# Kernel optimization log

Measured on AMD Instinct MI355X. Metric: run time of the kernel, lower is better.

Reference implementation:

```python
import jax, jax.numpy as jnp
import numpy as np

B, S, D, H, R = 2, 2048, 1024, 16, 4
HD = D // H  # 64


def _linear_params(key, din, dout):
    k1, k2 = jax.random.split(key)
    bound = 1.0 / np.sqrt(din)
    w = jax.random.uniform(k1, (din, dout), jnp.float32, -bound, bound)
    b = jax.random.uniform(k2, (dout,), jnp.float32, -bound, bound)
    return w, b


def setup_inputs() -> dict:
    key = jax.random.key(0)
    ks = jax.random.split(key, 10)
    x = jax.random.normal(ks[0], (B, S, D), jnp.float32)
    wq_p, bq_p = _linear_params(ks[1], D, D)
    wk_p, bk_p = _linear_params(ks[2], D, D)
    wv_p, bv_p = _linear_params(ks[3], D, D)
    wo_p, bo_p = _linear_params(ks[4], D, D)
    wq_s, bq_s = _linear_params(ks[5], D, H * R)
    wk_s, bk_s = _linear_params(ks[6], D, H * R)
    wv_s, bv_s = _linear_params(ks[7], D, H * R)
    wo_s, bo_s = _linear_params(ks[8], H * R, D)
    w_cross = jnp.float32(-0.1)
    return {"x": x,
            "wq_p": wq_p, "bq_p": bq_p, "wk_p": wk_p, "bk_p": bk_p,
            "wv_p": wv_p, "bv_p": bv_p, "wo_p": wo_p, "bo_p": bo_p,
            "wq_s": wq_s, "bq_s": bq_s, "wk_s": wk_s, "bk_s": bk_s,
            "wv_s": wv_s, "bv_s": bv_s, "wo_s": wo_s, "bo_s": bo_s,
            "w_cross": w_cross}


def _mha(x, wq, bq, wk, bk, wv, bv, dh, scale):
    b, s, _ = x.shape
    q = (x @ wq + bq).reshape(b, s, H, dh)
    k = (x @ wk + bk).reshape(b, s, H, dh)
    v = (x @ wv + bv).reshape(b, s, H, dh)
    scores = jnp.einsum('bqhd,bkhd->bhqk', q, k) / scale
    attn = jax.nn.softmax(scores, axis=-1)
    out = jnp.einsum('bhqk,bkhd->bqhd', attn, v)
    return out.reshape(b, s, H * dh)


def reference(x, wq_p, bq_p, wk_p, bk_p, wv_p, bv_p, wo_p, bo_p,
              wq_s, bq_s, wk_s, bk_s, wv_s, bv_s, wo_s, bo_s, w_cross):
    primary = _mha(x, wq_p, bq_p, wk_p, bk_p, wv_p, bv_p, HD, np.sqrt(HD)) @ wo_p + bo_p
    secondary = _mha(x, wq_s, bq_s, wk_s, bk_s, wv_s, bv_s, R, np.sqrt(R)) @ wo_s + bo_s
    return primary + w_cross * secondary
```

## Files before the change

### kernel.cpp

```cpp
#include <hip/hip_runtime.h>
#include <stdint.h>

typedef unsigned short u16;
typedef __bf16 bf16x8 __attribute__((ext_vector_type(8)));
typedef float f32x4 __attribute__((ext_vector_type(4)));
typedef u16 u16x8 __attribute__((ext_vector_type(8)));
typedef u16 u16x4 __attribute__((ext_vector_type(4)));
typedef unsigned u32x4 __attribute__((ext_vector_type(4)));


__device__ __forceinline__ u16 f2bf(float f) {
  unsigned u = __builtin_bit_cast(unsigned, f);
  u += 0x7FFFu + ((u >> 16) & 1u);
  return (u16)(u >> 16);
}
__device__ __forceinline__ unsigned cvtpk(float lo, float hi) {
  unsigned r;
  asm("v_cvt_pk_bf16_f32 %0, %1, %2" : "=v"(r) : "v"(lo), "v"(hi));
  return r;
}
__device__ __forceinline__ void gld_lds16(const void* g, void* l) {
  __builtin_amdgcn_global_load_lds((__attribute__((address_space(1))) void*)(g),
                                   (__attribute__((address_space(3))) void*)(l),
                                   16, 0, 0);
}

__global__ __launch_bounds__(256)
void k_prep(const float* __restrict__ x,
            const float* __restrict__ wq_p, const float* __restrict__ wk_p,
            const float* __restrict__ wv_p, const float* __restrict__ wo_p,
            const float* __restrict__ wq_s, const float* __restrict__ wk_s,
            const float* __restrict__ wv_s, const float* __restrict__ wo_s,
            const float* __restrict__ bq_p, const float* __restrict__ bk_p,
            const float* __restrict__ bq_s, const float* __restrict__ bk_s,
            const float* __restrict__ bo_p, const float* __restrict__ bo_s,
            const float* __restrict__ wcr,
            u16* __restrict__ xb, u16* __restrict__ Wall, u16* __restrict__ Wvt,
            u16* __restrict__ Wvst, u16* __restrict__ Bto,
            float* __restrict__ ballqk, float* __restrict__ bfin) {
  const int id = blockIdx.x;
  if (id < 2048) {
    const int i = id * 256 + threadIdx.x;
    const float4* p = reinterpret_cast<const float4*>(x) + (size_t)i * 2;
    float4 a = p[0], b = p[1];
    u16x8 o;
    o[0] = f2bf(a.x); o[1] = f2bf(a.y); o[2] = f2bf(a.z); o[3] = f2bf(a.w);
    o[4] = f2bf(b.x); o[5] = f2bf(b.y); o[6] = f2bf(b.z); o[7] = f2bf(b.w);
    *reinterpret_cast<u16x8*>(xb + (size_t)i * 8) = o;
    return;
  }
  if (id < 6400) {
    __shared__ float tile[32][33];
    const int tx = threadIdx.x & 31, ty = threadIdx.x >> 5;
    const float* src; u16* dst; int N, ldd, n0, k0; float sc = 1.f;
    if (id < 6144) {
      const int tid = id - 2048, job = tid >> 10, t10 = tid & 1023;
      switch (job) {
        case 0: src = wq_p; dst = Wall;                       ldd = 1024; break;
        case 1: src = wk_p; dst = Wall + (size_t)1024 * 1024; ldd = 1024; break;
        case 2: src = wv_p; dst = Wvt;                        ldd = 1024; break;
        default: src = wo_p; dst = Bto;                       ldd = 1088; break;
      }
      N = 1024; n0 = (t10 & 31) * 32; k0 = (t10 >> 5) * 32;
    } else {
      const int tid = id - 6144, job = tid >> 6, t6 = tid & 63;
      int ntx;
      switch (job) {
        case 0: src = wq_s; dst = Wall + (size_t)2048 * 1024; N = 64;   ldd = 1024; ntx = 2; break;
        case 1: src = wk_s; dst = Wall + (size_t)2112 * 1024; N = 64;   ldd = 1024; ntx = 2; break;
        case 2: src = wv_s; dst = Wvst;                       N = 64;   ldd = 1024; ntx = 2; break;
        default: src = wo_s; dst = Bto + 1024;                N = 1024; ldd = 1088; ntx = 32; sc = wcr[0]; break;
      }
      n0 = (t6 % ntx) * 32; k0 = (t6 / ntx) * 32;
    }
    #pragma unroll
    for (int i = 0; i < 4; ++i)
      tile[ty + i * 8][tx] = src[(size_t)(k0 + ty + i * 8) * N + n0 + tx];
    __syncthreads();
    #pragma unroll
    for (int i = 0; i < 4; ++i)
      dst[(size_t)(n0 + ty + i * 8) * ldd + k0 + tx] = f2bf(tile[tx][ty + i * 8] * sc);
    return;
  }
  const int i = (id - 6400) * 256 + threadIdx.x;
  if (i < 1024)       ballqk[i] = bq_p[i];
  else if (i < 2048)  ballqk[i] = bk_p[i - 1024];
  else if (i < 2112)  ballqk[i] = bq_s[i - 2048];
  else if (i < 2176)  ballqk[i] = bk_s[i - 2112];
  if (i < 1024) bfin[i] = bo_p[i] + wcr[0] * bo_s[i];
}

template <int BN, int WAVES_M, int OUTMODE, int OHD = 64>
__global__ __launch_bounds__(256, 2)
void k_gemm_bt(const u16* __restrict__ A, int lda,
               const u16* __restrict__ Bt, int ldb,
               const float* __restrict__ bias,
               void* __restrict__ Cv, int ldc, int K) {
  constexpr int WM = 128 / WAVES_M;
  constexpr int MF = WM / 16;
  __shared__ __attribute__((aligned(16))) u16 Atile[2][128 * 32];
  __shared__ __attribute__((aligned(16))) u16 Btile[2][BN * 32];
  const int t = threadIdx.x, w = t >> 6;
  const int lane = t & 63, l4 = lane & 15, g = lane >> 4;
  const int wr = (WAVES_M == 4) ? w : (w >> 1);
  const int wc = (WAVES_M == 4) ? 0 : (w & 1);
  const int m0 = blockIdx.x * 128, n0 = blockIdx.y * BN;

  auto stage = [&](int buf, int kt) {
    const int k0 = kt * 32;
    #pragma unroll
    for (int r = 0; r < 2; ++r) {
      const int slot = r * 256 + t;
      const int row = slot >> 2, blk = slot & 3;
      const int srcb = blk ^ ((row >> 1) & 3);
      gld_lds16(A + (size_t)(m0 + row) * lda + k0 + srcb * 8,
                &Atile[buf][(r * 256 + w * 64) * 8]);
    }
    #pragma unroll
    for (int r = 0; r < BN / 64; ++r) {
      const int slot = r * 256 + t;
      const int row = slot >> 2, blk = slot & 3;
      const int srcb = blk ^ ((row >> 1) & 3);
      gld_lds16(Bt + (size_t)(n0 + row) * ldb + k0 + srcb * 8,
                &Btile[buf][(r * 256 + w * 64) * 8]);
    }
  };

  const f32x4 vz = {0.f, 0.f, 0.f, 0.f};
  f32x4 acc[MF][4];
  #pragma unroll
  for (int mi = 0; mi < MF; ++mi)
    #pragma unroll
    for (int ni = 0; ni < 4; ++ni) acc[mi][ni] = vz;

  const int nkt = K >> 5;
  stage(0, 0);
  __syncthreads();
  for (int kt = 0; kt < nkt; ++kt) {
    const int cur = kt & 1;
    if (kt + 1 < nkt) stage(cur ^ 1, kt + 1);
    bf16x8 af[MF], bfv[4];
    #pragma unroll
    for (int mi = 0; mi < MF; ++mi) {
      const int row = wr * WM + mi * 16 + l4;
      const int blk = g ^ ((row >> 1) & 3);
      af[mi] = *reinterpret_cast<const bf16x8*>(&Atile[cur][row * 32 + blk * 8]);
    }
    #pragma unroll
    for (int ni = 0; ni < 4; ++ni) {
      const int row = wc * 64 + ni * 16 + l4;
      const int blk = g ^ ((row >> 1) & 3);
      bfv[ni] = *reinterpret_cast<const bf16x8*>(&Btile[cur][row * 32 + blk * 8]);
    }
    #pragma unroll
    for (int mi = 0; mi < MF; ++mi)
      #pragma unroll
      for (int ni = 0; ni < 4; ++ni)
        acc[mi][ni] = __builtin_amdgcn_mfma_f32_16x16x32_bf16(af[mi], bfv[ni],
                                                              acc[mi][ni], 0, 0, 0);
    __syncthreads();
  }
  #pragma unroll
  for (int mi = 0; mi < MF; ++mi) {
    #pragma unroll
    for (int ni = 0; ni < 4; ++ni) {
      const int grow0 = m0 + wr * WM + mi * 16 + g * 4;
      const int gcol = n0 + wc * 64 + ni * 16 + l4;
      const float bb = bias ? bias[gcol] : 0.f;
      if constexpr (OUTMODE == 1) {
        const int bidx = grow0 >> 11, s0 = grow0 & 2047;
        const int hh = gcol / OHD, dd = gcol % OHD;
        u16x4 ov;
        #pragma unroll
        for (int r = 0; r < 4; ++r) ov[r] = f2bf(acc[mi][ni][r] + bb);
        *reinterpret_cast<u16x4*>((u16*)Cv +
            (size_t)((bidx * 16 + hh) * OHD + dd) * 2048 + s0) = ov;
      } else {
        #pragma unroll
        for (int r = 0; r < 4; ++r) {
          const float v = acc[mi][ni][r] + bb;
          if constexpr (OUTMODE == 0)
            ((u16*)Cv)[(size_t)(grow0 + r) * ldc + gcol] = f2bf(v);
          else
            ((float*)Cv)[(size_t)(grow0 + r) * ldc + gcol] = v;
        }
      }
    }
  }
}

__global__ __launch_bounds__(256, 2)
void k_attn(const u16* __restrict__ QKs, const u16* __restrict__ Vpt,
            const u16* __restrict__ Vst, u16* __restrict__ Ao) {
  __shared__ __attribute__((aligned(16))) u16 sm[26664];
  const int t = threadIdx.x, w = t >> 6;
  const int lane = t & 63, l4 = lane & 15, g = lane >> 4;

  if (blockIdx.x < 512) {
    u16* Klds = sm;
    u16* Vlds = sm + 8192;
    const int id = blockIdx.x;
    const int lin = (id & 7) * 64 + (id >> 3);
    const int qt = lin & 15, hb = lin >> 4;
    const int h = hb & 15, b = hb >> 4;
    const int q0 = qt * 128;

    const u16* Qbase = QKs + (size_t)(b * 2048 + q0) * 2176 + h * 64;
    const u16* Kbase = QKs + (size_t)(b * 2048) * 2176 + 1024 + h * 64;
    const u16* Vbase = Vpt + (size_t)((b * 16 + h) * 64) * 2048;

    #pragma unroll
    for (int r = 0; r < 2; ++r) {
      const int sl = r * 256 + t, row = sl >> 3, blk = sl & 7;
      const int srcb = blk ^ (row & 7);
      const int prow = (row & 32) | (((row >> 2) & 3) << 3) | (((row >> 4) & 1) << 2) | (row & 3);
      gld_lds16(Kbase + (size_t)prow * 2176 + srcb * 8, &Klds[(r * 256 + w * 64) * 8]);
      gld_lds16(Vbase + (size_t)row * 2048 + srcb * 8, &Vlds[(r * 256 + w * 64) * 8]);
    }

    bf16x8 aq[2][2];
    #pragma unroll
    for (int mi = 0; mi < 2; ++mi)
      #pragma unroll
      for (int kd = 0; kd < 2; ++kd)
        aq[mi][kd] = *reinterpret_cast<const bf16x8*>(
            Qbase + (size_t)(w * 32 + mi * 16 + l4) * 2176 + kd * 32 + g * 8);

    __syncthreads();

    const f32x4 vz = {0.f, 0.f, 0.f, 0.f};
    float l_r[2] = {0.f, 0.f};
    f32x4 acc_o[2][4];
    #pragma unroll
    for (int mi = 0; mi < 2; ++mi)
      #pragma unroll
      for (int nd = 0; nd < 4; ++nd) acc_o[mi][nd] = vz;

    for (int kt = 0; kt < 32; ++kt) {
      const int cur = kt & 1;
      if (kt < 31) {
        const int kn = kt + 1;
        #pragma unroll
        for (int r = 0; r < 2; ++r) {
          const int sl = r * 256 + t, row = sl >> 3, blk = sl & 7;
          const int srcb = blk ^ (row & 7);
          const int prow = (row & 32) | (((row >> 2) & 3) << 3) | (((row >> 4) & 1) << 2) | (row & 3);
          gld_lds16(Kbase + (size_t)(kn * 64 + prow) * 2176 + srcb * 8,
                    &Klds[(cur ^ 1) * 4096 + (r * 256 + w * 64) * 8]);
          gld_lds16(Vbase + (size_t)row * 2048 + kn * 64 + srcb * 8,
                    &Vlds[(cur ^ 1) * 4096 + (r * 256 + w * 64) * 8]);
        }
      }
      f32x4 sc[2][4];
      #pragma unroll
      for (int mi = 0; mi < 2; ++mi)
        #pragma unroll
        for (int ni = 0; ni < 4; ++ni) sc[mi][ni] = vz;
      #pragma unroll
      for (int kd = 0; kd < 2; ++kd) {
        bf16x8 bk[4];
        #pragma unroll
        for (int ni = 0; ni < 4; ++ni) {
          const int row = ni * 16 + l4;
          const int blk = (kd * 4 + g) ^ (row & 7);
          bk[ni] = *reinterpret_cast<const bf16x8*>(&Klds[cur * 4096 + row * 64 + blk * 8]);
        }
        __builtin_amdgcn_s_setprio(1);
        #pragma unroll
        for (int mi = 0; mi < 2; ++mi)
          #pragma unroll
          for (int ni = 0; ni < 4; ++ni)
            sc[mi][ni] = __builtin_amdgcn_mfma_f32_16x16x32_bf16(bk[ni], aq[mi][kd],
                                                                 sc[mi][ni], 0, 0, 0);
        __builtin_amdgcn_s_setprio(0);
      }
      unsigned pw[2][4][2];
      #pragma unroll
      for (int mi = 0; mi < 2; ++mi) {
        float rs = 0.f;
        #pragma unroll
        for (int ni = 0; ni < 4; ++ni) {
          const float a0 = __expf(sc[mi][ni][0] * 0.125f);
          const float a1 = __expf(sc[mi][ni][1] * 0.125f);
          const float a2 = __expf(sc[mi][ni][2] * 0.125f);
          const float a3 = __expf(sc[mi][ni][3] * 0.125f);
          rs += (a0 + a1) + (a2 + a3);
          pw[mi][ni][0] = cvtpk(a0, a1);
          pw[mi][ni][1] = cvtpk(a2, a3);
        }
        rs += __shfl_xor(rs, 16);
        rs += __shfl_xor(rs, 32);
        l_r[mi] += rs;
      }
      #pragma unroll
      for (int ks = 0; ks < 2; ++ks) {
        bf16x8 bv[4];
        #pragma unroll
        for (int nd = 0; nd < 4; ++nd) {
          const int row = nd * 16 + l4;
          const int blk = (ks * 4 + g) ^ (row & 7);
          bv[nd] = *reinterpret_cast<const bf16x8*>(&Vlds[cur * 4096 + row * 64 + blk * 8]);
        }
        __builtin_amdgcn_s_setprio(1);
        #pragma unroll
        for (int mi = 0; mi < 2; ++mi) {
          const u32x4 aw = {pw[mi][2 * ks][0], pw[mi][2 * ks][1],
                            pw[mi][2 * ks + 1][0], pw[mi][2 * ks + 1][1]};
          const bf16x8 ap = __builtin_bit_cast(bf16x8, aw);
          #pragma unroll
          for (int nd = 0; nd < 4; ++nd)
            acc_o[mi][nd] = __builtin_amdgcn_mfma_f32_16x16x32_bf16(ap, bv[nd],
                                                                    acc_o[mi][nd], 0, 0, 0);
        }
        __builtin_amdgcn_s_setprio(0);
      }
      __syncthreads();
    }
    float linv[2][4];
    #pragma unroll
    for (int mi = 0; mi < 2; ++mi)
      #pragma unroll
      for (int r = 0; r < 4; ++r) {
        const int src = (lane & 48) + ((lane & 48) >> 2) + r;
        linv[mi][r] = 1.0f / __shfl(l_r[mi], src);
      }
    #pragma unroll
    for (int mi = 0; mi < 2; ++mi)
      #pragma unroll
      for (int nd = 0; nd < 4; ++nd)
        #pragma unroll
        for (int r = 0; r < 4; ++r) {
          const int grow = b * 2048 + q0 + w * 32 + mi * 16 + g * 4 + r;
          const int gcol = h * 64 + nd * 16 + l4;
          Ao[(size_t)grow * 1088 + gcol] = f2bf(acc_o[mi][nd][r] * linv[mi][r]);
        }
    return;
  }

  u16* KsL = sm;
  u16* VtL = sm + 8192;
  u16* Plds = sm + 18472;
  const int sid = blockIdx.x - 512;
  const int q0 = (sid & 15) * 128, h = (sid >> 4) & 15, b = sid >> 8;

  const u16* Vsrc = Vst + (size_t)((b * 16 + h) * 4) * 2048;
  #pragma unroll
  for (int r = 0; r < 4; ++r)
    gld_lds16(Vsrc + (size_t)r * 2048 + t * 8, &VtL[r * 2056 + w * 512]);
  {
    u16x8 ones;
    #pragma unroll
    for (int j = 0; j < 8; ++j) ones[j] = 0x3F80;
    *reinterpret_cast<u16x8*>(&VtL[4 * 2056 + t * 8]) = ones;
  }
  #pragma unroll
  for (int i = 0; i < 8; ++i) {
    const int s = i * 256 + t;
    const uint2 kk = *reinterpret_cast<const uint2*>(
        QKs + (size_t)(b * 2048 + s) * 2176 + 2112 + h * 4);
    *reinterpret_cast<uint2*>(&KsL[s * 4]) = kk;
  }
  bf16x8 aq[2];
  #pragma unroll
  for (int mi = 0; mi < 2; ++mi) {
    u16x8 qv = {0, 0, 0, 0, 0, 0, 0, 0};
    if (g == 0) {
      const uint2 qq = *reinterpret_cast<const uint2*>(
          QKs + (size_t)(b * 2048 + q0 + w * 32 + mi * 16 + l4) * 2176 + 2048 + h * 4);
      qv[0] = (u16)(qq.x & 0xffff); qv[1] = (u16)(qq.x >> 16);
      qv[2] = (u16)(qq.y & 0xffff); qv[3] = (u16)(qq.y >> 16);
    }
    aq[mi] = __builtin_bit_cast(bf16x8, qv);
  }
  __syncthreads();

  const f32x4 vz = {0.f, 0.f, 0.f, 0.f};
  f32x4 acc[2];
  acc[0] = vz; acc[1] = vz;

  for (int kt = 0; kt < 32; ++kt) {
    f32x4 sc[2][4];
    bf16x8 bk[4];
    #pragma unroll
    for (int ni = 0; ni < 4; ++ni) {
      u16x8 kv = {0, 0, 0, 0, 0, 0, 0, 0};
      if (g == 0) {
        const uint2 kk = *reinterpret_cast<const uint2*>(
            &KsL[(kt * 64 + ni * 16 + l4) * 4]);
        kv[0] = (u16)(kk.x & 0xffff); kv[1] = (u16)(kk.x >> 16);
        kv[2] = (u16)(kk.y & 0xffff); kv[3] = (u16)(kk.y >> 16);
      }
      bk[ni] = __builtin_bit_cast(bf16x8, kv);
    }
    #pragma unroll
    for (int mi = 0; mi < 2; ++mi)
      #pragma unroll
      for (int ni = 0; ni < 4; ++ni)
        sc[mi][ni] = __builtin_amdgcn_mfma_f32_16x16x32_bf16(aq[mi], bk[ni], vz, 0, 0, 0);
    #pragma unroll
    for (int mi = 0; mi < 2; ++mi)
      #pragma unroll
      for (int r = 0; r < 4; ++r) {
        const int prow = mi * 16 + g * 4 + r;
        #pragma unroll
        for (int ni = 0; ni < 4; ++ni) {
          const float p = __expf(sc[mi][ni][r] * 0.5f);
          const int col = ni * 16 + l4;
          Plds[w * 2048 + prow * 64 + ((col >> 3) ^ (prow & 7)) * 8 + (col & 7)] = f2bf(p);
        }
      }
  asm volatile("s_waitcnt lgkmcnt(0)" ::: "memory");
    #pragma unroll
    for (int ks = 0; ks < 2; ++ks) {
      const int blko = kt * 8 + ks * 4 + g;
      const int vrow = (l4 < 4) ? l4 : 4;
      const bf16x8 bv = *reinterpret_cast<const bf16x8*>(&VtL[vrow * 2056 + blko * 8]);
      #pragma unroll
      for (int mi = 0; mi < 2; ++mi) {
        const int row = mi * 16 + l4;
        const int blk = (ks * 4 + g) ^ (row & 7);
        const bf16x8 ap = *reinterpret_cast<const bf16x8*>(&Plds[w * 2048 + row * 64 + blk * 8]);
        acc[mi] = __builtin_amdgcn_mfma_f32_16x16x32_bf16(ap, bv, acc[mi], 0, 0, 0);
      }
    }
  }
  #pragma unroll
  for (int mi = 0; mi < 2; ++mi)
    #pragma unroll
    for (int r = 0; r < 4; ++r) {
      const float lsum = __shfl(acc[mi][r], (lane & 48) + 4);
      if (l4 < 4) {
        const int grow = b * 2048 + q0 + w * 32 + mi * 16 + g * 4 + r;
        Ao[(size_t)grow * 1088 + 1024 + h * 4 + l4] = f2bf(acc[mi][r] / lsum);
      }
    }
}

extern "C" void kernel_launch(void* const* d_in, const int* in_sizes, int n_in,
                              void* d_out, int out_size, void* d_ws, size_t ws_size,
                              hipStream_t stream) {
  (void)in_sizes; (void)n_in; (void)out_size; (void)ws_size;
  const float* x    = (const float*)d_in[0];
  const float* wq_p = (const float*)d_in[1];
  const float* bq_p = (const float*)d_in[2];
  const float* wk_p = (const float*)d_in[3];
  const float* bk_p = (const float*)d_in[4];
  const float* wv_p = (const float*)d_in[5];
  const float* bv_p = (const float*)d_in[6];
  const float* wo_p = (const float*)d_in[7];
  const float* bo_p = (const float*)d_in[8];
  const float* wq_s = (const float*)d_in[9];
  const float* bq_s = (const float*)d_in[10];
  const float* wk_s = (const float*)d_in[11];
  const float* bk_s = (const float*)d_in[12];
  const float* wv_s = (const float*)d_in[13];
  const float* bv_s = (const float*)d_in[14];
  const float* wo_s = (const float*)d_in[15];
  const float* bo_s = (const float*)d_in[16];
  const float* wcr  = (const float*)d_in[17];

  char* p = (char*)d_ws;
  auto take = [&](size_t bytes) { char* r = p; p += (bytes + 255) & ~(size_t)255; return r; };
  u16* xb      = (u16*)take((size_t)4096 * 1024 * 2);
  u16* Wall    = (u16*)take((size_t)2176 * 1024 * 2);
  u16* Wvt     = (u16*)take((size_t)1024 * 1024 * 2);
  u16* Wvst    = (u16*)take((size_t)64 * 1024 * 2);
  u16* Bto     = (u16*)take((size_t)1024 * 1088 * 2);
  float* ballqk= (float*)take(2176 * 4);
  float* bfin  = (float*)take(1024 * 4);
  u16* QKs     = (u16*)take((size_t)4096 * 2176 * 2);
  u16* Vpt     = (u16*)take((size_t)4096 * 1024 * 2);
  u16* Vst     = (u16*)take((size_t)2 * 16 * 4 * 2048 * 2);
  u16* Ao      = (u16*)take((size_t)4096 * 1088 * 2);

  k_prep<<<6409, 256, 0, stream>>>(x, wq_p, wk_p, wv_p, wo_p, wq_s, wk_s, wv_s, wo_s,
                                   bq_p, bk_p, bq_s, bk_s, bo_p, bo_s, wcr,
                                   xb, Wall, Wvt, Wvst, Bto, ballqk, bfin);

  k_gemm_bt<128, 2, 0><<<dim3(32, 17), 256, 0, stream>>>(xb, 1024, Wall, 1024, ballqk,
                                                         QKs, 2176, 1024);
  k_gemm_bt<128, 2, 1, 64><<<dim3(32, 8), 256, 0, stream>>>(xb, 1024, Wvt, 1024, bv_p, Vpt, 0, 1024);
  k_gemm_bt<64, 4, 1, 4><<<dim3(32, 1), 256, 0, stream>>>(xb, 1024, Wvst, 1024, bv_s, Vst, 0, 1024);

  k_attn<<<1024, 256, 0, stream>>>(QKs, Vpt, Vst, Ao);

  k_gemm_bt<128, 2, 2><<<dim3(32, 8), 256, 0, stream>>>(Ao, 1088, Bto, 1088, bfin, d_out, 1024, 1088);
}
```

Measured before the change: 188.3 us.

## Merge three projection GEMM launches into one kernel and interleave attention blocks

Measured after the change: 154.8 us. 1.22x faster.

```diff
diff --git a/kernel.cpp b/kernel.cpp
--- a/kernel.cpp
+++ b/kernel.cpp
@@ -90,21 +90,22 @@
   if (i < 1024) bfin[i] = bo_p[i] + wcr[0] * bo_s[i];
 }
 
-template <int BN, int WAVES_M, int OUTMODE, int OHD = 64>
-__global__ __launch_bounds__(256, 2)
-void k_gemm_bt(const u16* __restrict__ A, int lda,
+template <int BN, int WAVES_M, int OUTMODE, int OHD>
+__device__ __forceinline__
+void gemm_body(const u16* __restrict__ A, int lda,
                const u16* __restrict__ Bt, int ldb,
                const float* __restrict__ bias,
-               void* __restrict__ Cv, int ldc, int K) {
+               void* __restrict__ Cv, int ldc, int K,
+               int bx, int by, u16* sm) {
   constexpr int WM = 128 / WAVES_M;
   constexpr int MF = WM / 16;
-  __shared__ __attribute__((aligned(16))) u16 Atile[2][128 * 32];
-  __shared__ __attribute__((aligned(16))) u16 Btile[2][BN * 32];
+  u16* Atile = sm;
+  u16* Btile = sm + 8192;
   const int t = threadIdx.x, w = t >> 6;
   const int lane = t & 63, l4 = lane & 15, g = lane >> 4;
   const int wr = (WAVES_M == 4) ? w : (w >> 1);
   const int wc = (WAVES_M == 4) ? 0 : (w & 1);
-  const int m0 = blockIdx.x * 128, n0 = blockIdx.y * BN;
+  const int m0 = bx * 128, n0 = by * BN;
 
   auto stage = [&](int buf, int kt) {
     const int k0 = kt * 32;
@@ -114,7 +115,7 @@
       const int row = slot >> 2, blk = slot & 3;
       const int srcb = blk ^ ((row >> 1) & 3);
       gld_lds16(A + (size_t)(m0 + row) * lda + k0 + srcb * 8,
-                &Atile[buf][(r * 256 + w * 64) * 8]);
+                &Atile[buf * 4096 + (r * 256 + w * 64) * 8]);
     }
     #pragma unroll
     for (int r = 0; r < BN / 64; ++r) {
@@ -122,7 +123,7 @@
       const int row = slot >> 2, blk = slot & 3;
       const int srcb = blk ^ ((row >> 1) & 3);
       gld_lds16(Bt + (size_t)(n0 + row) * ldb + k0 + srcb * 8,
-                &Btile[buf][(r * 256 + w * 64) * 8]);
+                &Btile[buf * (BN * 32) + (r * 256 + w * 64) * 8]);
     }
   };
 
@@ -144,13 +145,13 @@
     for (int mi = 0; mi < MF; ++mi) {
       const int row = wr * WM + mi * 16 + l4;
       const int blk = g ^ ((row >> 1) & 3);
-      af[mi] = *reinterpret_cast<const bf16x8*>(&Atile[cur][row * 32 + blk * 8]);
+      af[mi] = *reinterpret_cast<const bf16x8*>(&Atile[cur * 4096 + row * 32 + blk * 8]);
     }
     #pragma unroll
     for (int ni = 0; ni < 4; ++ni) {
       const int row = wc * 64 + ni * 16 + l4;
       const int blk = g ^ ((row >> 1) & 3);
-      bfv[ni] = *reinterpret_cast<const bf16x8*>(&Btile[cur][row * 32 + blk * 8]);
+      bfv[ni] = *reinterpret_cast<const bf16x8*>(&Btile[cur * (BN * 32) + row * 32 + blk * 8]);
     }
     #pragma unroll
     for (int mi = 0; mi < MF; ++mi)
@@ -190,16 +191,47 @@
 }
 
 __global__ __launch_bounds__(256, 2)
+void k_proj3(const u16* __restrict__ xb, const u16* __restrict__ Wall,
+             const u16* __restrict__ Wvt, const u16* __restrict__ Wvst,
+             const float* __restrict__ ballqk, const float* __restrict__ bv_p,
+             const float* __restrict__ bv_s,
+             u16* __restrict__ QKs, u16* __restrict__ Vpt, u16* __restrict__ Vst) {
+  __shared__ __attribute__((aligned(16))) u16 sm[16384];
+  const int id = blockIdx.x;
+  if (id < 544) {
+    gemm_body<128, 2, 0, 64>(xb, 1024, Wall, 1024, ballqk, QKs, 2176, 1024,
+                             id & 31, id >> 5, sm);
+  } else if (id < 800) {
+    const int lid = id - 544;
+    gemm_body<128, 2, 1, 64>(xb, 1024, Wvt, 1024, bv_p, Vpt, 0, 1024,
+                             lid & 31, lid >> 5, sm);
+  } else {
+    const int lid = id - 800;
+    gemm_body<64, 4, 1, 4>(xb, 1024, Wvst, 1024, bv_s, Vst, 0, 1024,
+                           lid & 31, lid >> 5, sm);
+  }
+}
+
+__global__ __launch_bounds__(256, 2)
+void k_gemm_final(const u16* __restrict__ A, const u16* __restrict__ Bt,
+                  const float* __restrict__ bias, float* __restrict__ C) {
+  __shared__ __attribute__((aligned(16))) u16 sm[16384];
+  gemm_body<128, 2, 2, 64>(A, 1088, Bt, 1088, bias, C, 1024, 1088,
+                           blockIdx.x, blockIdx.y, sm);
+}
+
+__global__ __launch_bounds__(256, 2)
 void k_attn(const u16* __restrict__ QKs, const u16* __restrict__ Vpt,
             const u16* __restrict__ Vst, u16* __restrict__ Ao) {
   __shared__ __attribute__((aligned(16))) u16 sm[26664];
   const int t = threadIdx.x, w = t >> 6;
   const int lane = t & 63, l4 = lane & 15, g = lane >> 4;
-
-  if (blockIdx.x < 512) {
+  const int grp = blockIdx.x >> 3, sub = blockIdx.x & 7;
+
+  if ((grp & 1) == 0) {
     u16* Klds = sm;
     u16* Vlds = sm + 8192;
-    const int id = blockIdx.x;
+    const int id = (grp >> 1) * 8 + sub;
     const int lin = (id & 7) * 64 + (id >> 3);
     const int qt = lin & 15, hb = lin >> 4;
     const int h = hb & 15, b = hb >> 4;
@@ -340,7 +372,7 @@
   u16* KsL = sm;
   u16* VtL = sm + 8192;
   u16* Plds = sm + 18472;
-  const int sid = blockIdx.x - 512;
+  const int sid = (grp >> 1) * 8 + sub;
   const int q0 = (sid & 15) * 128, h = (sid >> 4) & 15, b = sid >> 8;
 
   const u16* Vsrc = Vst + (size_t)((b * 16 + h) * 4) * 2048;
@@ -409,7 +441,7 @@
           Plds[w * 2048 + prow * 64 + ((col >> 3) ^ (prow & 7)) * 8 + (col & 7)] = f2bf(p);
         }
       }
-  asm volatile("s_waitcnt lgkmcnt(0)" ::: "memory");
+    asm volatile("s_waitcnt lgkmcnt(0)" ::: "memory");
     #pragma unroll
     for (int ks = 0; ks < 2; ++ks) {
       const int blko = kt * 8 + ks * 4 + g;
@@ -477,12 +509,10 @@
                                    bq_p, bk_p, bq_s, bk_s, bo_p, bo_s, wcr,
                                    xb, Wall, Wvt, Wvst, Bto, ballqk, bfin);
 
-  k_gemm_bt<128, 2, 0><<<dim3(32, 17), 256, 0, stream>>>(xb, 1024, Wall, 1024, ballqk,
-                                                         QKs, 2176, 1024);
-  k_gemm_bt<128, 2, 1, 64><<<dim3(32, 8), 256, 0, stream>>>(xb, 1024, Wvt, 1024, bv_p, Vpt, 0, 1024);
-  k_gemm_bt<64, 4, 1, 4><<<dim3(32, 1), 256, 0, stream>>>(xb, 1024, Wvst, 1024, bv_s, Vst, 0, 1024);
+  k_proj3<<<832, 256, 0, stream>>>(xb, Wall, Wvt, Wvst, ballqk, bv_p, bv_s,
+                                   QKs, Vpt, Vst);
 
   k_attn<<<1024, 256, 0, stream>>>(QKs, Vpt, Vst, Ao);
 
-  k_gemm_bt<128, 2, 2><<<dim3(32, 8), 256, 0, stream>>>(Ao, 1088, Bto, 1088, bfin, d_out, 1024, 1088);
-}
+  k_gemm_final<<<dim3(32, 8), 256, 0, stream>>>(Ao, Bto, bfin, (float*)d_out);
+}
```
